# Performance work log

Hardware: AMD Instinct MI355X
Metric: run time of the kernel (lower is better)

The kernel has to match this reference:

```python
import jax, jax.numpy as jnp
import numpy as np

HB, WB = 200, 200
X_MIN, X_MAX = -50.0, 50.0
Y_MIN, Y_MAX = -50.0, 50.0


def _nearest_resize(x, Hp, Wp):
    # torch F.interpolate(mode='nearest'): src = floor(dst * in/out)
    Hs, Ws = x.shape[-2], x.shape[-1]
    iy = (jnp.arange(Hp) * (Hs / Hp)).astype(jnp.int32)
    ix = (jnp.arange(Wp) * (Ws / Wp)).astype(jnp.int32)
    return x[..., iy[:, None], ix[None, :]]


def _make_extrinsics(B, T, C):
    # per-camera yaw around ego z, composed with axis permutation ego->cam
    P = np.array([[0.0, -1.0, 0.0], [0.0, 0.0, -1.0], [1.0, 0.0, 0.0]], np.float32)
    mats = np.zeros((C, 4, 4), np.float32)
    for c in range(C):
        a = 2.0 * np.pi * c / C
        Rz = np.array([[np.cos(a), -np.sin(a), 0.0], [np.sin(a), np.cos(a), 0.0], [0.0, 0.0, 1.0]], np.float32)
        mats[c, :3, :3] = P @ Rz
        mats[c, :3, 3] = np.array([0.1 * c, -0.05 * c, 1.5], np.float32)
        mats[c, 3, 3] = 1.0
    return jnp.broadcast_to(jnp.asarray(mats), (B, T, C, 4, 4))


def setup_inputs() -> dict:
    key = jax.random.key(0)
    k1, k2 = jax.random.split(key)
    B, T, C, Cr, Hp, Wp = 2, 2, 6, 64, 32, 88
    H, W = 256, 704
    feats = jax.random.normal(k1, (B, T, C, Cr, Hp, Wp), dtype=jnp.float32)
    depths = jax.random.uniform(k2, (B, T, C, H, W), dtype=jnp.float32) * 59.0 + 1.0
    K = jnp.array([[557.0, 0.0, 352.0], [0.0, 557.0, 128.0], [0.0, 0.0, 1.0]], jnp.float32)
    K_scaled = jnp.broadcast_to(K, (B, T, C, 3, 3))
    T_cam_from_ego = _make_extrinsics(B, T, C)
    return {"feats": feats, "depths": depths, "K_scaled": K_scaled,
            "T_cam_from_ego": T_cam_from_ego, "H": H, "W": W}


def reference(feats, depths, K_scaled, T_cam_from_ego, H, W):
    B, T, C, Cr, Hp, Wp = feats.shape
    rx = (X_MAX - X_MIN) / float(WB)
    ry = (Y_MAX - Y_MIN) / float(HB)
    d = _nearest_resize(depths, Hp, Wp)  # [B,T,C,Hp,Wp]
    # scale intrinsics from (H,W) to (Hp,Wp)
    Sy, Sx = Hp / float(H), Wp / float(W)
    scale = jnp.array([[Sx, 1.0, Sx], [1.0, Sy, Sy], [1.0, 1.0, 1.0]], feats.dtype)
    Kp = K_scaled * scale
    T_ego_from_cam = jnp.linalg.inv(T_cam_from_ego)  # [B,T,C,4,4]
    uu = jnp.arange(Wp, dtype=feats.dtype)[None, :]  # broadcast over Hp
    vv = jnp.arange(Hp, dtype=feats.dtype)[:, None]
    fx = Kp[..., 0, 0][..., None, None]
    fy = Kp[..., 1, 1][..., None, None]
    cx = Kp[..., 0, 2][..., None, None]
    cy = Kp[..., 1, 2][..., None, None]
    x_c = (uu - cx) / fx * d
    y_c = (vv - cy) / fy * d
    Xc = jnp.stack([x_c, y_c, d, jnp.ones_like(d)], axis=3)  # [B,T,C,4,Hp,Wp]
    Xe = jnp.einsum('btcij,btcjhw->btcihw', T_ego_from_cam[..., 0:3, :], Xc)
    x = Xe[:, :, :, 0]
    y = Xe[:, :, :, 1]
    valid = (d > 0) & (x >= X_MIN) & (x < X_MAX) & (y >= Y_MIN) & (y < Y_MAX)
    ix = jnp.clip(jnp.floor((x - X_MIN) / rx), 0, WB - 1).astype(jnp.int32)
    iy = jnp.clip(jnp.floor((y - Y_MIN) / ry), 0, HB - 1).astype(jnp.int32)
    lin = iy * WB + ix  # [B,T,C,Hp,Wp]
    idx = jnp.where(valid, lin, 0)
    N, P = B * T * C, Hp * Wp
    seg = (jnp.arange(N, dtype=jnp.int32)[:, None] * (HB * WB) + idx.reshape(N, P)).reshape(-1)
    w = valid.reshape(N, 1, P).astype(feats.dtype)
    vals = (feats.reshape(N, Cr, P) * w).transpose(0, 2, 1).reshape(N * P, Cr)
    out = jax.ops.segment_sum(vals, seg, num_segments=N * HB * WB)  # [N*HB*WB, Cr]
    cnt = jax.ops.segment_sum(w.reshape(-1), seg, num_segments=N * HB * WB)
    out = out.reshape(B, T, C, HB * WB, Cr)
    cnt = cnt.reshape(B, T, C, HB * WB)
    num = out.sum(axis=2)                                  # [B,T,HB*WB,Cr]
    den = jnp.maximum(cnt, 1.0).sum(axis=2)                # [B,T,HB*WB]
    res = num / den[..., None]
    return res.transpose(0, 1, 3, 2).reshape(B, T, Cr, HB, WB)
```

## Files before the change

### kernel.cpp

```cpp
#include <hip/hip_runtime.h>

constexpr int B  = 2, T = 2, C = 6, Cr = 64, Hp = 32, Wp = 88;
constexpr int H  = 256, W = 704;
constexpr int HB = 200, WB = 200;
constexpr int NB   = B * T * C;
constexpr int BT   = B * T;
constexpr int P    = Hp * Wp;
constexpr int NBIN = HB * WB;
constexpr int PTS_BT = C * P;

constexpr float X_MIN = -50.f, Y_MIN = -50.f;

constexpr int TB    = 128;
constexpr int TILES = (NBIN + TB - 1) / TB;

constexpr size_t CNT_ELEMS  = (size_t)NB * NBIN;
constexpr size_t BIDX_ELEMS = (size_t)NB * P;
constexpr size_t RDEN_ELEMS = (size_t)BT * NBIN;
constexpr size_t FT_ELEMS   = (size_t)NB * P * Cr;
constexpr size_t CNT_BYTES  = CNT_ELEMS * 4;
constexpr size_t BIDX_BYTES = BIDX_ELEMS * 4;
constexpr size_t RDEN_BYTES = RDEN_ELEMS * 4;

__global__ void geom_kernel(const float* __restrict__ depths,
                            const float* __restrict__ Kmat,
                            const float* __restrict__ Tmat,
                            int* __restrict__ binidx,
                            int* __restrict__ cnt) {
    const int n = blockIdx.y;
    const int p = blockIdx.x * blockDim.x + threadIdx.x;
    const int v = p / Wp, u = p % Wp;

    const float* Kp = Kmat + n * 9;
    const float* M  = Tmat + n * 16;

    const float Sx = (float)Wp / (float)W;
    const float Sy = (float)Hp / (float)H;
    const float fx = Kp[0] * Sx, cx = Kp[2] * Sx;
    const float fy = Kp[4] * Sy, cy = Kp[5] * Sy;

    const float r00 = M[0], t0 = M[3];
    const float r10 = M[4], t1 = M[7];
    const float r20 = M[8], t2 = M[11];
    const float r01 = M[1], r11 = M[5], r21 = M[9];
    const float ti0 = -(r00 * t0 + r10 * t1 + r20 * t2);
    const float ti1 = -(r01 * t0 + r11 * t1 + r21 * t2);

    const float d = depths[(size_t)n * H * W + (size_t)(v * (H / Hp)) * W + u * (W / Wp)];

    const float xc = ((float)u - cx) / fx * d;
    const float yc = ((float)v - cy) / fy * d;
    const float x  = r00 * xc + r10 * yc + r20 * d + ti0;
    const float y  = r01 * xc + r11 * yc + r21 * d + ti1;

    const bool valid = (d > 0.f) && (x >= X_MIN) && (x < -X_MIN) &&
                       (y >= Y_MIN) && (y < -Y_MIN);
    int bin = -1;
    if (valid) {
        const float ixf = floorf((x - X_MIN) * 2.f);
        const float iyf = floorf((y - Y_MIN) * 2.f);
        const int ix = (int)fminf(fmaxf(ixf, 0.f), (float)(WB - 1));
        const int iy = (int)fminf(fmaxf(iyf, 0.f), (float)(HB - 1));
        bin = iy * WB + ix;
        atomicAdd(&cnt[n * NBIN + bin], 1);
    }
    binidx[n * P + p] = bin;
}

__global__ void rden_kernel(const int* __restrict__ cnt,
                            float* __restrict__ rden) {
    const int g   = blockIdx.x * blockDim.x + threadIdx.x;
    const int bt  = g / NBIN;
    const int bin = g % NBIN;
    float den = 0.f;
#pragma unroll
    for (int c = 0; c < C; ++c) {
        const int cc = cnt[(bt * C + c) * NBIN + bin];
        den += (float)(cc > 1 ? cc : 1);
    }
    rden[g] = 1.f / den;
}

__global__ void transpose_kernel(const float* __restrict__ feats,
                                 float* __restrict__ feats_t) {
    __shared__ float tile[64][65];
    const int n  = blockIdx.y;
    const int p0 = blockIdx.x * 64;
    const int tp = threadIdx.x & 63;
    const int tq = threadIdx.x >> 6;

    const float* src = feats + (size_t)n * Cr * P + p0;
#pragma unroll
    for (int k = 0; k < 16; ++k) {
        const int cr = k * 4 + tq;
        tile[cr][tp] = src[(size_t)cr * P + tp];
    }
    __syncthreads();
    float* dst = feats_t + ((size_t)n * P + p0) * Cr;
#pragma unroll
    for (int k = 0; k < 16; ++k) {
        const int p = k * 4 + tq;
        dst[(size_t)p * Cr + tp] = tile[tp][p];
    }
}

__global__ void accum_kernel(const float* __restrict__ feats_t,
                             const int* __restrict__ binidx,
                             const float* __restrict__ rden,
                             float* __restrict__ out) {
    __shared__ float acc[TB * 64];
    const int bt = blockIdx.y;
    const int lo = blockIdx.x * TB;

    for (int i = threadIdx.x; i < TB * 64; i += 256) acc[i] = 0.f;
    __syncthreads();

    const int lane = threadIdx.x & 63;
    const int wave = threadIdx.x >> 6;
    const int* bi      = binidx + (size_t)bt * PTS_BT;
    const float* ft    = feats_t + (size_t)bt * PTS_BT * Cr;

    const int seg = PTS_BT / 4;
    for (int base = wave * seg; base < (wave + 1) * seg; base += 64) {
        const int b = bi[base + lane];
        const bool match = (b >= lo) && (b < lo + TB);
        unsigned long long mask = __ballot(match);
        while (mask) {
            const int bit = __ffsll(mask) - 1;
            mask &= mask - 1;
            const int bm = __shfl(b, bit);
            const int im = base + bit;
            const float v = ft[(size_t)im * Cr + lane];
            atomicAdd(&acc[(bm - lo) * 64 + (lane ^ (bm & 31))], v);
        }
    }
    __syncthreads();

    const int bl  = threadIdx.x & (TB - 1);
    const int bin = lo + bl;
    if (bin < NBIN) {
        const float r = rden[(size_t)bt * NBIN + bin];
        const int cr0 = (threadIdx.x >> 7) * 32;
        float* ob = out + (size_t)bt * Cr * NBIN + bin;
#pragma unroll
        for (int k = 0; k < 32; ++k) {
            const int cr = cr0 + k;
            ob[(size_t)cr * NBIN] = acc[bl * 64 + (cr ^ (bl & 31))] * r;
        }
    }
}

extern "C" void kernel_launch(void* const* d_in, const int* in_sizes, int n_in,
                              void* d_out, int out_size, void* d_ws, size_t ws_size,
                              hipStream_t stream) {
    const float* feats  = (const float*)d_in[0];
    const float* depths = (const float*)d_in[1];
    const float* Kmat   = (const float*)d_in[2];
    const float* Tmat   = (const float*)d_in[3];

    int*   cnt     = (int*)d_ws;
    int*   binidx  = (int*)((char*)d_ws + CNT_BYTES);
    float* rden    = (float*)((char*)d_ws + CNT_BYTES + BIDX_BYTES);
    float* feats_t = (float*)((char*)d_ws + CNT_BYTES + BIDX_BYTES + RDEN_BYTES);
    float* out     = (float*)d_out;

    hipMemsetAsync(cnt, 0, CNT_BYTES, stream);

    geom_kernel<<<dim3(P / 256, NB), 256, 0, stream>>>(depths, Kmat, Tmat, binidx, cnt);
    rden_kernel<<<(BT * NBIN) / 256, 256, 0, stream>>>(cnt, rden);
    transpose_kernel<<<dim3(P / 64, NB), 256, 0, stream>>>(feats, feats_t);
    accum_kernel<<<dim3(TILES, BT), 256, 0, stream>>>(feats_t, binidx, rden, out);
}
```

Before: 162.9 us.

## Bucket points by bin tile with counting sort instead of full rescans

Before, every accumulate block scanned all points of its batch-time slice and ballot-matched the ones falling in its 128-bin tile, so total work scaled with tiles times points. Now geom counts points per 64-bin tile, a single-block scan builds offsets, and a fill kernel scatters packed point records into per-tile buckets. Each accumulate block then reads only its own bucket. The reciprocal-denominator kernel is folded into accum's epilogue. This costs two extra small launches, a serial single-block scan, and global atomics on the bucket cursors.

```diff
diff --git a/kernel.cpp b/kernel.cpp
--- a/kernel.cpp
+++ b/kernel.cpp
@@ -11,22 +11,23 @@
 
 constexpr float X_MIN = -50.f, Y_MIN = -50.f;
 
-constexpr int TB    = 128;
-constexpr int TILES = (NBIN + TB - 1) / TB;
-
-constexpr size_t CNT_ELEMS  = (size_t)NB * NBIN;
-constexpr size_t BIDX_ELEMS = (size_t)NB * P;
-constexpr size_t RDEN_ELEMS = (size_t)BT * NBIN;
-constexpr size_t FT_ELEMS   = (size_t)NB * P * Cr;
-constexpr size_t CNT_BYTES  = CNT_ELEMS * 4;
-constexpr size_t BIDX_BYTES = BIDX_ELEMS * 4;
-constexpr size_t RDEN_BYTES = RDEN_ELEMS * 4;
+constexpr int TB     = 64;
+constexpr int TILES  = NBIN / TB;
+constexpr int NBUCK  = BT * TILES;
+
+constexpr size_t CNT_BYTES   = (size_t)NB * NBIN * 4;
+constexpr size_t TCNT_BYTES  = (size_t)NBUCK * 4;
+constexpr size_t OFF_BYTES   = (size_t)NBUCK * 4;
+constexpr size_t CUR_BYTES   = (size_t)NBUCK * 4;
+constexpr size_t BIDX_BYTES  = (size_t)NB * P * 4;
+constexpr size_t REC_BYTES   = (size_t)NB * P * 4;
 
 __global__ void geom_kernel(const float* __restrict__ depths,
                             const float* __restrict__ Kmat,
                             const float* __restrict__ Tmat,
                             int* __restrict__ binidx,
-                            int* __restrict__ cnt) {
+                            int* __restrict__ cnt,
+                            int* __restrict__ tilecnt) {
     const int n = blockIdx.y;
     const int p = blockIdx.x * blockDim.x + threadIdx.x;
     const int v = p / Wp, u = p % Wp;
@@ -63,22 +64,57 @@
         const int iy = (int)fminf(fmaxf(iyf, 0.f), (float)(HB - 1));
         bin = iy * WB + ix;
         atomicAdd(&cnt[n * NBIN + bin], 1);
+        atomicAdd(&tilecnt[(n / C) * TILES + (bin >> 6)], 1);
     }
     binidx[n * P + p] = bin;
 }
 
-__global__ void rden_kernel(const int* __restrict__ cnt,
-                            float* __restrict__ rden) {
-    const int g   = blockIdx.x * blockDim.x + threadIdx.x;
-    const int bt  = g / NBIN;
-    const int bin = g % NBIN;
-    float den = 0.f;
-#pragma unroll
-    for (int c = 0; c < C; ++c) {
-        const int cc = cnt[(bt * C + c) * NBIN + bin];
-        den += (float)(cc > 1 ? cc : 1);
-    }
-    rden[g] = 1.f / den;
+__global__ void scan_kernel(const int* __restrict__ tilecnt,
+                            int* __restrict__ off,
+                            int* __restrict__ cursor) {
+    __shared__ int part[256];
+    const int t = threadIdx.x;
+    constexpr int CH = (NBUCK + 255) / 256;
+    int pre[CH];
+    int s = 0;
+#pragma unroll
+    for (int k = 0; k < CH; ++k) {
+        const int i = t * CH + k;
+        pre[k] = s;
+        if (i < NBUCK) s += tilecnt[i];
+    }
+    part[t] = s;
+    __syncthreads();
+    for (int dlt = 1; dlt < 256; dlt <<= 1) {
+        const int v = (t >= dlt) ? part[t - dlt] : 0;
+        __syncthreads();
+        part[t] += v;
+        __syncthreads();
+    }
+    const int excl = (t == 0) ? 0 : part[t - 1];
+#pragma unroll
+    for (int k = 0; k < CH; ++k) {
+        const int i = t * CH + k;
+        if (i < NBUCK) {
+            const int o = excl + pre[k];
+            off[i] = o;
+            cursor[i] = o;
+        }
+    }
+}
+
+__global__ void fill_kernel(const int* __restrict__ binidx,
+                            int* __restrict__ cursor,
+                            int* __restrict__ rec) {
+    const int n = blockIdx.y;
+    const int p = blockIdx.x * blockDim.x + threadIdx.x;
+    const int b = binidx[n * P + p];
+    if (b >= 0) {
+        const int bt  = n / C;
+        const int pbt = (n % C) * P + p;
+        const int pos = atomicAdd(&cursor[bt * TILES + (b >> 6)], 1);
+        rec[pos] = (pbt << 6) | (b & 63);
+    }
 }
 
 __global__ void transpose_kernel(const float* __restrict__ feats,
@@ -105,48 +141,48 @@
 }
 
 __global__ void accum_kernel(const float* __restrict__ feats_t,
-                             const int* __restrict__ binidx,
-                             const float* __restrict__ rden,
+                             const int* __restrict__ rec,
+                             const int* __restrict__ off,
+                             const int* __restrict__ cursor,
+                             const int* __restrict__ cnt,
                              float* __restrict__ out) {
     __shared__ float acc[TB * 64];
-    const int bt = blockIdx.y;
-    const int lo = blockIdx.x * TB;
+    const int bt   = blockIdx.y;
+    const int tile = blockIdx.x;
+    const int lo   = tile * TB;
 
     for (int i = threadIdx.x; i < TB * 64; i += 256) acc[i] = 0.f;
     __syncthreads();
 
     const int lane = threadIdx.x & 63;
     const int wave = threadIdx.x >> 6;
-    const int* bi      = binidx + (size_t)bt * PTS_BT;
-    const float* ft    = feats_t + (size_t)bt * PTS_BT * Cr;
-
-    const int seg = PTS_BT / 4;
-    for (int base = wave * seg; base < (wave + 1) * seg; base += 64) {
-        const int b = bi[base + lane];
-        const bool match = (b >= lo) && (b < lo + TB);
-        unsigned long long mask = __ballot(match);
-        while (mask) {
-            const int bit = __ffsll(mask) - 1;
-            mask &= mask - 1;
-            const int bm = __shfl(b, bit);
-            const int im = base + bit;
-            const float v = ft[(size_t)im * Cr + lane];
-            atomicAdd(&acc[(bm - lo) * 64 + (lane ^ (bm & 31))], v);
-        }
-    }
-    __syncthreads();
-
-    const int bl  = threadIdx.x & (TB - 1);
-    const int bin = lo + bl;
-    if (bin < NBIN) {
-        const float r = rden[(size_t)bt * NBIN + bin];
-        const int cr0 = (threadIdx.x >> 7) * 32;
-        float* ob = out + (size_t)bt * Cr * NBIN + bin;
-#pragma unroll
-        for (int k = 0; k < 32; ++k) {
-            const int cr = cr0 + k;
-            ob[(size_t)cr * NBIN] = acc[bl * 64 + (cr ^ (bl & 31))] * r;
-        }
+    const int bucket = bt * TILES + tile;
+    const int start = off[bucket];
+    const int end   = cursor[bucket];
+    const float* f  = feats_t + (size_t)bt * PTS_BT * Cr;
+
+    for (int j = start + wave; j < end; j += 4) {
+        const int r  = rec[j];
+        const int bl = r & 63;
+        const int p  = r >> 6;
+        const float v = f[(size_t)p * Cr + lane];
+        atomicAdd(&acc[bl * 64 + (lane ^ (bl & 31))], v);
+    }
+    __syncthreads();
+
+    const int bin = lo + lane;
+    float den = 0.f;
+#pragma unroll
+    for (int c = 0; c < C; ++c) {
+        const int cc = cnt[(bt * C + c) * NBIN + bin];
+        den += (float)(cc > 1 ? cc : 1);
+    }
+    const float rden = 1.f / den;
+    float* ob = out + (size_t)bt * Cr * NBIN + bin;
+#pragma unroll
+    for (int k = 0; k < 16; ++k) {
+        const int cr = wave * 16 + k;
+        ob[(size_t)cr * NBIN] = acc[lane * 64 + (cr ^ (lane & 31))] * rden;
     }
 }
 
@@ -158,16 +194,23 @@
     const float* Kmat   = (const float*)d_in[2];
     const float* Tmat   = (const float*)d_in[3];
 
-    int*   cnt     = (int*)d_ws;
-    int*   binidx  = (int*)((char*)d_ws + CNT_BYTES);
-    float* rden    = (float*)((char*)d_ws + CNT_BYTES + BIDX_BYTES);
-    float* feats_t = (float*)((char*)d_ws + CNT_BYTES + BIDX_BYTES + RDEN_BYTES);
+    char* w = (char*)d_ws;
+    int*   cnt     = (int*)w;                      w += CNT_BYTES;
+    int*   tilecnt = (int*)w;                      w += TCNT_BYTES;
+    int*   off     = (int*)w;                      w += OFF_BYTES;
+    int*   cursor  = (int*)w;                      w += CUR_BYTES;
+    int*   binidx  = (int*)w;                      w += BIDX_BYTES;
+    int*   rec     = (int*)w;                      w += REC_BYTES;
+    float* feats_t = (float*)w;
     float* out     = (float*)d_out;
 
-    hipMemsetAsync(cnt, 0, CNT_BYTES, stream);
-
-    geom_kernel<<<dim3(P / 256, NB), 256, 0, stream>>>(depths, Kmat, Tmat, binidx, cnt);
-    rden_kernel<<<(BT * NBIN) / 256, 256, 0, stream>>>(cnt, rden);
+    hipMemsetAsync(cnt, 0, CNT_BYTES + TCNT_BYTES, stream);
+
+    geom_kernel<<<dim3(P / 256, NB), 256, 0, stream>>>(depths, Kmat, Tmat,
+                                                       binidx, cnt, tilecnt);
+    scan_kernel<<<1, 256, 0, stream>>>(tilecnt, off, cursor);
+    fill_kernel<<<dim3(P / 256, NB), 256, 0, stream>>>(binidx, cursor, rec);
     transpose_kernel<<<dim3(P / 64, NB), 256, 0, stream>>>(feats, feats_t);
-    accum_kernel<<<dim3(TILES, BT), 256, 0, stream>>>(feats_t, binidx, rden, out);
-}
+    accum_kernel<<<dim3(TILES, BT), 256, 0, stream>>>(feats_t, rec, off,
+                                                      cursor, cnt, out);
+}
```

New measurement: 164.5 us. No clear change (+1.0%).
